# Performance work log

Hardware: AMD Instinct MI355X
Metric: run time of the kernel (lower is better)

The kernel has to match this reference:

```python
import jax, jax.numpy as jnp
import numpy as np

N_EXPERTS = 8
TOP_K = 2


def setup_inputs() -> dict:
    key = jax.random.key(0)
    k1, k2, k3, k4 = jax.random.split(key, 4)
    B, T, C, H, E = 2, 2048, 1024, 4096, N_EXPERTS
    x = jax.random.normal(k1, (B, T, C), dtype=jnp.float32)
    # weights scaled like standard init to keep activations well-behaved
    router_w = jax.random.normal(k2, (E, C), dtype=jnp.float32) * 0.02
    w1 = jax.random.normal(k3, (E, C, H), dtype=jnp.float32) * (1.0 / np.sqrt(C))
    w2 = jax.random.normal(k4, (E, H, C), dtype=jnp.float32) * (1.0 / np.sqrt(H))
    return {"x": x, "router_w": router_w, "w1": w1, "w2": w2}


def reference(x, router_w, w1, w2):
    B, T, C = x.shape
    E = N_EXPERTS
    xf = x.reshape(-1, C)                                   # [N, C], N = B*T
    logits = jnp.einsum('nc,ec->ne', xf, router_w)          # router (no bias)
    probs = jax.nn.softmax(logits, axis=-1)
    top_w, top_i = jax.lax.top_k(probs, TOP_K)              # [N, K]
    top_w = top_w / jnp.sum(top_w, axis=-1, keepdims=True)  # renormalize
    # combine weight per (token, expert): sum of top-k weights routed to e
    comb = jnp.einsum('nk,nke->ne', top_w, jax.nn.one_hot(top_i, E, dtype=xf.dtype))
    # dense all-expert compute (bias=False, exact GELU, dropout=0 at eval)
    h = jax.nn.gelu(jnp.einsum('nc,ech->enh', xf, w1), approximate=False)  # [E, N, H]
    y = jnp.einsum('enh,ehc->enc', h, w2)                   # [E, N, C]
    out = jnp.einsum('ne,enc->nc', comb, y)                 # weighted combine
    return out.reshape(B, T, C)
```

## Files before the change

kernel.cpp:

```cpp
#include <hip/hip_runtime.h>
#include <hip/hip_bf16.h>
#include <stdint.h>

#define NTOK 4096
#define CD   1024
#define HD   4096
#define NE   8

typedef __attribute__((ext_vector_type(8))) short bf16x8;
typedef __attribute__((ext_vector_type(4))) float f32x4;
typedef __attribute__((ext_vector_type(4))) unsigned short us4;
typedef __attribute__((ext_vector_type(8))) unsigned short us8;

#define BARR() asm volatile("s_barrier" ::: "memory")
#define VM2() asm volatile("s_waitcnt vmcnt(2)" ::: "memory")
#define VM0() asm volatile("s_waitcnt vmcnt(0)" ::: "memory")

__device__ __forceinline__ unsigned short f2bf(float f){
  __hip_bfloat16 h = __float2bfloat16(f);
  return *reinterpret_cast<unsigned short*>(&h);
}

__global__ __launch_bounds__(256) void fused_pre(
    const float* __restrict__ x, const float* __restrict__ rw,
    const float* __restrict__ w1, const float* __restrict__ w2,
    unsigned short* __restrict__ x_bf, int* __restrict__ top_i,
    float* __restrict__ top_w, int* __restrict__ counts,
    unsigned short* __restrict__ w1t, unsigned short* __restrict__ w2t){
  __shared__ char smem_raw[33536];
  int bid = blockIdx.x;
  int tid = threadIdx.x;

  if (bid < NTOK/4){
    float* rw_lds = (float*)smem_raw;
    for (int i = tid; i < NE*CD/4; i += 256)
      ((float4*)rw_lds)[i] = ((const float4*)rw)[i];
    __syncthreads();
    int l = tid & 63, w = tid >> 6;
    int n = bid*4 + w;

    float4 xv[4];
    #pragma unroll
    for (int j = 0; j < 4; ++j)
      xv[j] = ((const float4*)(x + (size_t)n*CD))[l + j*64];

    #pragma unroll
    for (int j = 0; j < 4; ++j){
      us4 o; o.x = f2bf(xv[j].x); o.y = f2bf(xv[j].y); o.z = f2bf(xv[j].z); o.w = f2bf(xv[j].w);
      *(us4*)(x_bf + (size_t)n*CD + l*4 + j*256) = o;
    }

    double le[NE];
    #pragma unroll
    for (int e = 0; e < NE; ++e){
      double p = 0.0;
      #pragma unroll
      for (int j = 0; j < 4; ++j){
        float4 rv = ((const float4*)(rw_lds + e*CD))[l + j*64];
        p += (double)xv[j].x*rv.x + (double)xv[j].y*rv.y + (double)xv[j].z*rv.z + (double)xv[j].w*rv.w;
      }
      #pragma unroll
      for (int d = 32; d >= 1; d >>= 1) p += __shfl_xor(p, d);
      le[e] = p;
    }
    if (l == 0){
      double m = le[0];
      #pragma unroll
      for (int e = 1; e < NE; ++e) m = le[e] > m ? le[e] : m;
      double pe[NE];
      #pragma unroll
      for (int e = 0; e < NE; ++e) pe[e] = exp(le[e]-m);
      int i0 = 0;
      #pragma unroll
      for (int e = 1; e < NE; ++e) if (pe[e] > pe[i0]) i0 = e;
      int i1 = (i0 == 0) ? 1 : 0;
      #pragma unroll
      for (int e = 0; e < NE; ++e){ if (e == i0) continue; if (pe[e] > pe[i1]) i1 = e; }
      double w0 = pe[i0], w1v = pe[i1], wsum = w0 + w1v;
      top_i[2*n] = i0; top_i[2*n+1] = i1;
      top_w[2*n] = (float)(w0/wsum); top_w[2*n+1] = (float)(w1v/wsum);
      atomicAdd(&counts[i0], 1); atomicAdd(&counts[i1], 1);
    }
    return;
  }

  typedef float ftile_t[64][65];
  ftile_t* tiles = (ftile_t*)smem_raw;
  bool isW1 = bid < NTOK/4 + 2048;
  int base = (isW1 ? (bid - NTOK/4) : (bid - NTOK/4 - 2048)) * 4;
  const float* W  = isW1 ? w1 : w2;
  unsigned short* Wt = isW1 ? w1t : w2t;
  const int R = isW1 ? CD : HD;
  const int S = isW1 ? HD : CD;

  int rr = tid >> 4, c4 = tid & 15;
  int ss8 = tid >> 3, rq8 = tid & 7;

  auto decode = [&](int t, int& s0, int& r0, size_t& eoff){
    int xx, yy, e;
    if (isW1){ xx = t & 63; yy = (t >> 6) & 15; e = t >> 10; }
    else     { xx = t & 15; yy = (t >> 4) & 63; e = t >> 10; }
    s0 = xx*64; r0 = yy*64; eoff = (size_t)e*CD*HD;
  };

  float4 v[4];
  auto LOADREGS = [&](int t){
    int s0, r0; size_t eoff; decode(t, s0, r0, eoff);
    const float* ip = W + eoff;
    #pragma unroll
    for (int i = 0; i < 4; ++i)
      v[i] = *(const float4*)(ip + (size_t)(r0 + i*16 + rr)*S + s0 + c4*4);
  };

  LOADREGS(base);
  #pragma unroll 1
  for (int it = 0; it < 4; ++it){
    float (*tile)[65] = tiles[it & 1];
    #pragma unroll
    for (int i = 0; i < 4; ++i){
      tile[i*16+rr][c4*4+0] = v[i].x; tile[i*16+rr][c4*4+1] = v[i].y;
      tile[i*16+rr][c4*4+2] = v[i].z; tile[i*16+rr][c4*4+3] = v[i].w;
    }
    if (it < 3) LOADREGS(base + it + 1);
    __syncthreads();
    int s0, r0; size_t eoff; decode(base + it, s0, r0, eoff);
    unsigned short* op = Wt + eoff;
    #pragma unroll
    for (int i2 = 0; i2 < 2; ++i2){
      int ss = i2*32 + ss8;
      us8 o;
      #pragma unroll
      for (int j = 0; j < 8; ++j)
        o[j] = f2bf(tile[rq8*8+j][ss]);
      *(us8*)(op + (size_t)(s0+ss)*R + r0 + rq8*8) = o;
    }
  }
}

__global__ void scan_kernel(const int* __restrict__ counts, int* __restrict__ offsets, int* __restrict__ cursor){
  if (threadIdx.x == 0){
    int s = 0;
    for (int e = 0; e < NE; ++e){ offsets[e] = s; cursor[e] = s; s += counts[e]; }
  }
}

__global__ __launch_bounds__(256) void scatter_kernel(
    const int* __restrict__ top_i, const float* __restrict__ top_w,
    int* __restrict__ cursor, int* __restrict__ g_tok, float* __restrict__ g_w){
  int n = blockIdx.x*256 + threadIdx.x;
  #pragma unroll
  for (int k = 0; k < 2; ++k){
    int e = top_i[2*n+k];
    int pos = atomicAdd(&cursor[e], 1);
    g_tok[pos] = n;
    g_w[pos] = top_w[2*n+k];
  }
}

template<int KLEN, int SPLITK, int EPI>
__global__ __launch_bounds__(512, 6) void gemm_ring3(
    const unsigned short* __restrict__ A_src,
    const unsigned short* __restrict__ B_src,
    unsigned short* __restrict__ h_out,
    float* __restrict__ outp,
    const int* __restrict__ g_tok,
    const float* __restrict__ g_w,
    const int* __restrict__ counts,
    const int* __restrict__ offsets,
    int NDIM, int KSTRIDE){
  constexpr int NT = KLEN/32;
  constexpr int ZPX = (NE*SPLITK)/8;
  __shared__ alignas(128) char lds[49152];

  int GN = gridDim.x, GY = gridDim.y;
  int p  = blockIdx.x + GN*(blockIdx.y + GY*blockIdx.z);
  int k8 = p & 7;
  int i  = p >> 3;
  int s  = i / (GN*GY);
  int r  = i - s*(GN*GY);
  int y  = r % GY;
  int xb = r / GY;
  int z  = k8*ZPX + s;

  int e  = (SPLITK == 1) ? z : (z / SPLITK);
  int kz = (SPLITK == 1) ? 0 : (z % SPLITK);
  int n_e = counts[e];
  int m0 = y*128;
  if (m0 >= n_e) return;
  int n0 = xb*128;
  int g_base = offsets[e];
  int kstart = kz*KLEN;

  int tid = threadIdx.x, l = tid & 63, w = tid >> 6;
  int wr = w >> 2, wc = w & 3;
  int lrow = l & 15, q = l >> 4;

  const unsigned short* src[2];
  uint32_t dst[2];
  #pragma unroll
  for (int ii = 0; ii < 2; ++ii){
    int g = ii*512 + tid;
    bool isA = g < 512;
    int gg = isA ? g : (g - 512);
    int row = gg >> 2, c = gg & 3;
    int cs = c ^ (row & 3) ^ ((row >> 2) & 3);
    if (isA){
      int rg = m0 + row; if (rg > n_e-1) rg = n_e-1;
      size_t arow;
      if (EPI == 0) arow = (size_t)g_tok[g_base + rg];
      else          arow = (size_t)(g_base + rg);
      src[ii] = A_src + arow*(size_t)KSTRIDE + kstart + cs*8;
    } else {
      src[ii] = B_src + ((size_t)e*NDIM + n0 + row)*(size_t)KSTRIDE + kstart + cs*8;
    }
    dst[ii] = (uint32_t)g*16u;
  }

  auto STAGE = [&](int tt, uint32_t bufoff){
    #pragma unroll
    for (int ii = 0; ii < 2; ++ii)
      __builtin_amdgcn_global_load_lds(
        (const __attribute__((address_space(1))) void*)(src[ii] + (size_t)tt*32),
        (__attribute__((address_space(3))) void*)&lds[dst[ii] + bufoff], 16, 0, 0);
  };

  uint32_t a_off[4], b_off[2];
  #pragma unroll
  for (int m = 0; m < 4; ++m){
    int ra = wr*64 + m*16 + lrow;
    int Xa = (ra & 3) ^ ((ra >> 2) & 3);
    a_off[m] = (uint32_t)(ra*64) + 16u*(uint32_t)(q ^ Xa);
  }
  #pragma unroll
  for (int n = 0; n < 2; ++n){
    int rb = wc*32 + n*16 + lrow;
    int Xb = (rb & 3) ^ ((rb >> 2) & 3);
    b_off[n] = 8192u + (uint32_t)(rb*64) + 16u*(uint32_t)(q ^ Xb);
  }

  f32x4 acc[4][2] = {};

  STAGE(0, 0u); STAGE(1, 16384u);

  uint32_t ro = 0u;
  uint32_t so = 32768u;
  #pragma unroll 1
  for (int kt = 0; kt < NT; ++kt){
    if (kt < NT-1) { VM2(); } else { VM0(); }
    BARR();
    if (kt + 2 < NT) STAGE(kt + 2, so);
    bf16x8 av[4], bv[2];
    #pragma unroll
    for (int m = 0; m < 4; ++m)
      av[m] = *(const bf16x8*)&lds[a_off[m] + ro];
    #pragma unroll
    for (int n = 0; n < 2; ++n)
      bv[n] = *(const bf16x8*)&lds[b_off[n] + ro];
    __builtin_amdgcn_s_setprio(1);
    #pragma unroll
    for (int m = 0; m < 4; ++m)
      #pragma unroll
      for (int n = 0; n < 2; ++n)
        acc[m][n] = __builtin_amdgcn_mfma_f32_16x16x32_bf16(av[m], bv[n], acc[m][n], 0, 0, 0);
    __builtin_amdgcn_s_setprio(0);
    ro = (ro == 32768u) ? 0u : ro + 16384u;
    so = (so == 32768u) ? 0u : so + 16384u;
  }

  if (EPI == 0){
    #pragma unroll
    for (int m = 0; m < 4; ++m){
      #pragma unroll
      for (int jj = 0; jj < 4; ++jj){
        int rr = m0 + wr*64 + m*16 + q*4 + jj;
        if (rr < n_e){
          unsigned short* hp = h_out + (size_t)(g_base + rr)*NDIM + n0 + wc*32 + lrow;
          #pragma unroll
          for (int n = 0; n < 2; ++n){
            float v = acc[m][n][jj];
            v = 0.5f*v*(1.0f + erff(v*0.70710678118654752f));
            hp[n*16] = f2bf(v);
          }
        }
      }
    }
  } else {
    #pragma unroll
    for (int m = 0; m < 4; ++m){
      #pragma unroll
      for (int jj = 0; jj < 4; ++jj){
        int rr = m0 + wr*64 + m*16 + q*4 + jj;
        if (rr < n_e){
          int slot = g_base + rr;
          int tt = g_tok[slot];
          float wgt = g_w[slot];
          float* op = outp + (size_t)tt*NDIM + n0 + wc*32 + lrow;
          #pragma unroll
          for (int n = 0; n < 2; ++n)
            atomicAdd(op + n*16, wgt*acc[m][n][jj]);
        }
      }
    }
  }
}

extern "C" void kernel_launch(void* const* d_in, const int* in_sizes, int n_in,
                              void* d_out, int out_size, void* d_ws, size_t ws_size,
                              hipStream_t stream) {
  const float* x  = (const float*)d_in[0];
  const float* rw = (const float*)d_in[1];
  const float* w1 = (const float*)d_in[2];
  const float* w2 = (const float*)d_in[3];

  size_t off = 0;
  auto alloc = [&](size_t sz) -> char* {
    char* p = (char*)d_ws + off;
    off += (sz + 255) & ~(size_t)255;
    return p;
  };
  unsigned short* x_bf = (unsigned short*)alloc((size_t)NTOK*CD*2);
  unsigned short* w1t  = (unsigned short*)alloc((size_t)NE*CD*HD*2);
  unsigned short* w2t  = (unsigned short*)alloc((size_t)NE*CD*HD*2);
  unsigned short* hbuf = (unsigned short*)alloc((size_t)NTOK*2*HD*2);
  int*   top_i  = (int*)alloc(NTOK*2*4);
  float* top_w  = (float*)alloc(NTOK*2*4);
  int*   counts = (int*)alloc(64);
  int*   offs   = (int*)alloc(64);
  int*   cursor = (int*)alloc(64);
  int*   g_tok  = (int*)alloc(NTOK*2*4);
  float* g_w    = (float*)alloc(NTOK*2*4);
  (void)ws_size; (void)in_sizes; (void)n_in; (void)out_size;

  hipMemsetAsync(d_out, 0, (size_t)NTOK*CD*4, stream);
  hipMemsetAsync(counts, 0, 64, stream);

  fused_pre<<<dim3(NTOK/4 + 2048 + 2048), dim3(256), 0, stream>>>(
      x, rw, w1, w2, x_bf, top_i, top_w, counts, w1t, w2t);
  scan_kernel<<<dim3(1), dim3(64), 0, stream>>>(counts, offs, cursor);
  scatter_kernel<<<dim3(NTOK/256), dim3(256), 0, stream>>>(top_i, top_w, cursor, g_tok, g_w);

  gemm_ring3<CD, 1, 0><<<dim3(HD/128, 12, NE), dim3(512), 0, stream>>>(
      x_bf, w1t, hbuf, (float*)nullptr, g_tok, g_w, counts, offs, HD, CD);
  gemm_ring3<HD/2, 2, 1><<<dim3(CD/128, 12, NE*2), dim3(512), 0, stream>>>(
      hbuf, w2t, (unsigned short*)nullptr, (float*)d_out, g_tok, g_w, counts, offs, CD, HD);
}
```

Before: 454.7 us.

## Fuse w2 transpose-convert into first expert GEMM launch to overlap with compute

Moves the fp32-to-bf16 transpose of w2 out of the preprocessing kernel and into the first grouped GEMM launch. The grid is interleaved so that of every 40 blocks, 24 do GEMM tiles and 16 do w2 conversion. The aim is to overlap the memory-bound weight conversion with the compute-bound GEMM instead of running it serially beforehand. In exchange, the conversion blocks share the GEMM's launch bounds, LDS allocation and occupancy, and GEMM blocks that exit early leave holes in the interleave.

Measured after the change: 453.5 us. No clear change (-0.3%).

```diff
diff --git a/kernel.cpp b/kernel.cpp
--- a/kernel.cpp
+++ b/kernel.cpp
@@ -23,10 +23,10 @@
 
 __global__ __launch_bounds__(256) void fused_pre(
     const float* __restrict__ x, const float* __restrict__ rw,
-    const float* __restrict__ w1, const float* __restrict__ w2,
+    const float* __restrict__ w1,
     unsigned short* __restrict__ x_bf, int* __restrict__ top_i,
     float* __restrict__ top_w, int* __restrict__ counts,
-    unsigned short* __restrict__ w1t, unsigned short* __restrict__ w2t){
+    unsigned short* __restrict__ w1t){
   __shared__ char smem_raw[33536];
   int bid = blockIdx.x;
   int tid = threadIdx.x;
@@ -86,30 +86,22 @@
 
   typedef float ftile_t[64][65];
   ftile_t* tiles = (ftile_t*)smem_raw;
-  bool isW1 = bid < NTOK/4 + 2048;
-  int base = (isW1 ? (bid - NTOK/4) : (bid - NTOK/4 - 2048)) * 4;
-  const float* W  = isW1 ? w1 : w2;
-  unsigned short* Wt = isW1 ? w1t : w2t;
-  const int R = isW1 ? CD : HD;
-  const int S = isW1 ? HD : CD;
-
+  int base = (bid - NTOK/4) * 4;
   int rr = tid >> 4, c4 = tid & 15;
   int ss8 = tid >> 3, rq8 = tid & 7;
 
   auto decode = [&](int t, int& s0, int& r0, size_t& eoff){
-    int xx, yy, e;
-    if (isW1){ xx = t & 63; yy = (t >> 6) & 15; e = t >> 10; }
-    else     { xx = t & 15; yy = (t >> 4) & 63; e = t >> 10; }
+    int xx = t & 63, yy = (t >> 6) & 15, e = t >> 10;
     s0 = xx*64; r0 = yy*64; eoff = (size_t)e*CD*HD;
   };
 
   float4 v[4];
   auto LOADREGS = [&](int t){
     int s0, r0; size_t eoff; decode(t, s0, r0, eoff);
-    const float* ip = W + eoff;
+    const float* ip = w1 + eoff;
     #pragma unroll
     for (int i = 0; i < 4; ++i)
-      v[i] = *(const float4*)(ip + (size_t)(r0 + i*16 + rr)*S + s0 + c4*4);
+      v[i] = *(const float4*)(ip + (size_t)(r0 + i*16 + rr)*HD + s0 + c4*4);
   };
 
   LOADREGS(base);
@@ -124,7 +116,7 @@
     if (it < 3) LOADREGS(base + it + 1);
     __syncthreads();
     int s0, r0; size_t eoff; decode(base + it, s0, r0, eoff);
-    unsigned short* op = Wt + eoff;
+    unsigned short* op = w1t + eoff;
     #pragma unroll
     for (int i2 = 0; i2 < 2; ++i2){
       int ss = i2*32 + ss8;
@@ -132,7 +124,7 @@
       #pragma unroll
       for (int j = 0; j < 8; ++j)
         o[j] = f2bf(tile[rq8*8+j][ss]);
-      *(us8*)(op + (size_t)(s0+ss)*R + r0 + rq8*8) = o;
+      *(us8*)(op + (size_t)(s0+ss)*CD + r0 + rq8*8) = o;
     }
   }
 }
@@ -157,7 +149,7 @@
   }
 }
 
-template<int KLEN, int SPLITK, int EPI>
+template<int KLEN, int SPLITK, int EPI, int FUSE>
 __global__ __launch_bounds__(512, 6) void gemm_ring3(
     const unsigned short* __restrict__ A_src,
     const unsigned short* __restrict__ B_src,
@@ -167,13 +159,61 @@
     const float* __restrict__ g_w,
     const int* __restrict__ counts,
     const int* __restrict__ offsets,
-    int NDIM, int KSTRIDE){
+    int NDIM, int KSTRIDE, int GN, int GY,
+    const float* __restrict__ w2src, unsigned short* __restrict__ w2dst){
   constexpr int NT = KLEN/32;
   constexpr int ZPX = (NE*SPLITK)/8;
   __shared__ alignas(128) char lds[49152];
 
-  int GN = gridDim.x, GY = gridDim.y;
-  int p  = blockIdx.x + GN*(blockIdx.y + GY*blockIdx.z);
+  int bid = blockIdx.x + gridDim.x*(blockIdx.y + gridDim.y*blockIdx.z);
+  int tid = threadIdx.x;
+  int p;
+  if (FUSE){
+    int gp = bid/40, rm = bid%40;
+    if (rm >= 24){
+      typedef float ftile_t[64][65];
+      ftile_t* tiles = (ftile_t*)lds;
+      int base = (gp*16 + (rm - 24)) * 4;
+      float4 v[2];
+      auto LOADREGS = [&](int t){
+        int xx = t & 15, yy = (t >> 4) & 63, e = t >> 10;
+        const float* ip = w2src + (size_t)e*CD*HD;
+        #pragma unroll
+        for (int i = 0; i < 2; ++i){
+          int lin = i*512 + tid;
+          v[i] = *(const float4*)(ip + (size_t)(yy*64 + (lin>>4))*CD + xx*64 + (lin&15)*4);
+        }
+      };
+      LOADREGS(base);
+      #pragma unroll 1
+      for (int it = 0; it < 4; ++it){
+        float (*tile)[65] = tiles[it & 1];
+        #pragma unroll
+        for (int i = 0; i < 2; ++i){
+          int lin = i*512 + tid;
+          int rr2 = lin >> 4, c4 = lin & 15;
+          tile[rr2][c4*4+0] = v[i].x; tile[rr2][c4*4+1] = v[i].y;
+          tile[rr2][c4*4+2] = v[i].z; tile[rr2][c4*4+3] = v[i].w;
+        }
+        if (it < 3) LOADREGS(base + it + 1);
+        __syncthreads();
+        int t = base + it;
+        int xx = t & 15, yy = (t >> 4) & 63, e = t >> 10;
+        unsigned short* op = w2dst + (size_t)e*CD*HD;
+        int ss = tid >> 3, rq8 = tid & 7;
+        us8 o;
+        #pragma unroll
+        for (int j = 0; j < 8; ++j)
+          o[j] = f2bf(tile[rq8*8+j][ss]);
+        *(us8*)(op + (size_t)(xx*64+ss)*HD + yy*64 + rq8*8) = o;
+      }
+      return;
+    }
+    p = gp*24 + rm;
+  } else {
+    p = bid;
+  }
+
   int k8 = p & 7;
   int i  = p >> 3;
   int s  = i / (GN*GY);
@@ -191,7 +231,7 @@
   int g_base = offsets[e];
   int kstart = kz*KLEN;
 
-  int tid = threadIdx.x, l = tid & 63, w = tid >> 6;
+  int l = tid & 63, w = tid >> 6;
   int wr = w >> 2, wc = w & 3;
   int lrow = l & 15, q = l >> 4;
 
@@ -334,13 +374,14 @@
   hipMemsetAsync(d_out, 0, (size_t)NTOK*CD*4, stream);
   hipMemsetAsync(counts, 0, 64, stream);
 
-  fused_pre<<<dim3(NTOK/4 + 2048 + 2048), dim3(256), 0, stream>>>(
-      x, rw, w1, w2, x_bf, top_i, top_w, counts, w1t, w2t);
+  fused_pre<<<dim3(NTOK/4 + 2048), dim3(256), 0, stream>>>(
+      x, rw, w1, x_bf, top_i, top_w, counts, w1t);
   scan_kernel<<<dim3(1), dim3(64), 0, stream>>>(counts, offs, cursor);
   scatter_kernel<<<dim3(NTOK/256), dim3(256), 0, stream>>>(top_i, top_w, cursor, g_tok, g_w);
 
-  gemm_ring3<CD, 1, 0><<<dim3(HD/128, 12, NE), dim3(512), 0, stream>>>(
-      x_bf, w1t, hbuf, (float*)nullptr, g_tok, g_w, counts, offs, HD, CD);
-  gemm_ring3<HD/2, 2, 1><<<dim3(CD/128, 12, NE*2), dim3(512), 0, stream>>>(
-      hbuf, w2t, (unsigned short*)nullptr, (float*)d_out, g_tok, g_w, counts, offs, CD, HD);
-}
+  gemm_ring3<CD, 1, 0, 1><<<dim3(5120), dim3(512), 0, stream>>>(
+      x_bf, w1t, hbuf, (float*)nullptr, g_tok, g_w, counts, offs, HD, CD, 32, 12, w2, w2t);
+  gemm_ring3<HD/2, 2, 1, 0><<<dim3(8, 12, 16), dim3(512), 0, stream>>>(
+      hbuf, w2t, (unsigned short*)nullptr, (float*)d_out, g_tok, g_w, counts, offs, CD, HD, 8, 12,
+      (const float*)nullptr, (unsigned short*)nullptr);
+}
```
